# Kernel optimization log

Hardware: AMD Instinct MI355X
Metric: run time of the kernel (lower is better)

## Reference

```python
import jax, jax.numpy as jnp
import numpy as np

N_NODES = 200000
IN_SIZE = 128
OUT_SIZE = 128
N_EDGES = 600000


def setup_inputs() -> dict:
    key = jax.random.key(0)
    k1, k2, k3, k4 = jax.random.split(key, 4)
    embedding = jax.random.normal(k1, (N_NODES, IN_SIZE), dtype=jnp.float32)
    up2down_edge_index = jax.random.randint(k2, (2, N_EDGES), 0, N_NODES, dtype=jnp.int64)
    # GCNConv params (glorot weight, zero bias as in PyG defaults)
    scale = np.sqrt(6.0 / (IN_SIZE + OUT_SIZE)).astype(np.float32)
    W = jax.random.uniform(k3, (IN_SIZE, OUT_SIZE), dtype=jnp.float32, minval=-scale, maxval=scale)
    b = jnp.zeros((OUT_SIZE,), dtype=jnp.float32)
    return {"embedding": embedding, "up2down_edge_index": up2down_edge_index, "W": W, "b": b}


def reference(embedding, up2down_edge_index, W, b):
    # PyG GCNConv: add self-loops, symmetric normalization, linear transform,
    # scatter-sum aggregation, add bias.
    N = embedding.shape[0]
    loops = jnp.arange(N, dtype=up2down_edge_index.dtype)
    src = jnp.concatenate([up2down_edge_index[0], loops])  # message sources
    dst = jnp.concatenate([up2down_edge_index[1], loops])  # message targets

    # degree of each target node (edge_weight = 1)
    deg = jax.ops.segment_sum(jnp.ones_like(src, dtype=embedding.dtype), dst, num_segments=N)
    deg_inv_sqrt = jnp.where(deg > 0, jax.lax.rsqrt(jnp.maximum(deg, 1.0)), 0.0)
    norm = deg_inv_sqrt[src] * deg_inv_sqrt[dst]  # [E+N]

    h = embedding @ W  # [N, out]
    msg = h[src] * norm[:, None]  # gather + scale, [E+N, out]
    out = jax.ops.segment_sum(msg, dst, num_segments=N)  # scatter-add
    return out + b
```

## Files before the change

kernel.cpp:

```cpp
#include <hip/hip_runtime.h>
#include <hip/hip_bf16.h>
#include <stdint.h>

typedef __attribute__((ext_vector_type(8))) short short8v;
typedef __attribute__((ext_vector_type(4))) float f32x4;

__device__ __forceinline__ unsigned short f2bf(float f) {
  unsigned int u = __float_as_uint(f);
  u += 0x7fffu + ((u >> 16) & 1u);
  return (unsigned short)(u >> 16);
}
__device__ __forceinline__ unsigned int pack2bf(float a, float b) {
  return (unsigned int)f2bf(a) | ((unsigned int)f2bf(b) << 16);
}
__device__ __forceinline__ float bf_lo(unsigned int v) { return __uint_as_float(v << 16); }
__device__ __forceinline__ float bf_hi(unsigned int v) { return __uint_as_float(v & 0xffff0000u); }

__global__ void k_count(const int* __restrict__ dst, int* deg, int E) {
  int e = blockIdx.x * blockDim.x + threadIdx.x;
  if (e < E) atomicAdd(&deg[dst[e]], 1);
}

__global__ void k_blocksum(const int* __restrict__ deg, int* partials, float* dis, int N) {
  __shared__ int s[256];
  int t = threadIdx.x;
  int i = blockIdx.x * 256 + t;
  int c = (i < N) ? deg[i] : 0;
  if (i < N) dis[i] = rsqrtf((float)(c + 1));
  s[t] = c;
  __syncthreads();
  for (int off = 128; off > 0; off >>= 1) {
    if (t < off) s[t] += s[t + off];
    __syncthreads();
  }
  if (t == 0) partials[blockIdx.x] = s[0];
}

__global__ void k_scan_partials(int* partials, int nb) {
  __shared__ int s[1024];
  int t = threadIdx.x;
  s[t] = (t < nb) ? partials[t] : 0;
  __syncthreads();
  for (int off = 1; off < 1024; off <<= 1) {
    int v = (t >= off) ? s[t - off] : 0;
    __syncthreads();
    s[t] += v;
    __syncthreads();
  }
  if (t < nb) partials[t] = (t == 0) ? 0 : s[t - 1];
}

__global__ void k_scan_final(const int* __restrict__ deg, const int* __restrict__ partials,
                             int* csr_off, int N, int E) {
  __shared__ int s[256];
  int t = threadIdx.x;
  int i = blockIdx.x * 256 + t;
  int c = (i < N) ? deg[i] : 0;
  s[t] = c;
  __syncthreads();
  for (int off = 1; off < 256; off <<= 1) {
    int v = (t >= off) ? s[t - off] : 0;
    __syncthreads();
    s[t] += v;
    __syncthreads();
  }
  if (i < N) csr_off[i] = partials[blockIdx.x] + s[t] - c;
  if (i == 0) csr_off[N] = E;
}

__global__ void k_fill(const int* __restrict__ src, const int* __restrict__ dst,
                       const int* __restrict__ csr_off, int* cursor, int* csr_src, int E) {
  int e = blockIdx.x * blockDim.x + threadIdx.x;
  if (e < E) {
    int d = dst[e];
    int p = atomicAdd(&cursor[d], 1);
    csr_src[csr_off[d] + p] = src[e];
  }
}

__global__ void k_wprep(const float* __restrict__ W, unsigned short* __restrict__ Wfrag) {
  int t = blockIdx.x * 256 + threadIdx.x;
  int j = t & 7;
  int lane = (t >> 3) & 63;
  int ktct = t >> 9;
  int kt = ktct & 3, ct = ktct >> 2;
  int col = ct * 16 + (lane & 15);
  int k = kt * 32 + 4 * (lane >> 4) + (j & 3) + 16 * (j >> 2);
  Wfrag[t] = f2bf(W[k * 128 + col]);
}

__device__ __forceinline__ short8v pack8(float4 a, float4 b) {
  short8v r;
  r[0] = (short)f2bf(a.x); r[1] = (short)f2bf(a.y);
  r[2] = (short)f2bf(a.z); r[3] = (short)f2bf(a.w);
  r[4] = (short)f2bf(b.x); r[5] = (short)f2bf(b.y);
  r[6] = (short)f2bf(b.z); r[7] = (short)f2bf(b.w);
  return r;
}

__global__ __launch_bounds__(256) void k_gemm3(const float* __restrict__ X,
     const unsigned short* __restrict__ Wfrag, const float* __restrict__ dis,
     unsigned short* __restrict__ hs, int N) {
  __shared__ unsigned short Wl[16384];
  int t = threadIdx.x;
  #pragma unroll
  for (int q = 0; q < 8; ++q)
    ((uint4*)Wl)[q * 256 + t] = ((const uint4*)Wfrag)[q * 256 + t];
  __syncthreads();

  int wv = t >> 6, lane = t & 63;
  int lr = lane & 15, lg = lane >> 4;
  int row = blockIdx.x * 64 + wv * 16 + lr;

  short8v afr[4];
  if (row < N) {
    const float* xp = X + (size_t)row * 128 + 4 * lg;
    #pragma unroll
    for (int kt = 0; kt < 4; ++kt) {
      float4 v0 = *(const float4*)(xp + kt * 32);
      float4 v1 = *(const float4*)(xp + kt * 32 + 16);
      afr[kt] = pack8(v0, v1);
    }
  } else {
    #pragma unroll
    for (int kt = 0; kt < 4; ++kt) {
      float4 z = {0.f, 0.f, 0.f, 0.f};
      afr[kt] = pack8(z, z);
    }
  }
  float d = (row < N) ? dis[row] : 0.f;

  #pragma unroll
  for (int ct = 0; ct < 8; ++ct) {
    f32x4 acc = {0.f, 0.f, 0.f, 0.f};
    #pragma unroll
    for (int kt = 0; kt < 4; ++kt) {
      short8v wfr = *(const short8v*)(Wl + (((ct * 4 + kt) * 64 + lane) * 8));
      acc = __builtin_amdgcn_mfma_f32_16x16x32_bf16(wfr, afr[kt], acc, 0, 0, 0);
    }
    if (row < N) {
      uint2 uu;
      uu.x = pack2bf(acc[0] * d, acc[1] * d);
      uu.y = pack2bf(acc[2] * d, acc[3] * d);
      *(uint2*)(hs + (size_t)row * 128 + ct * 16 + 4 * lg) = uu;
    }
  }
}

__device__ __forceinline__ void acc8(float* a, uint4 g) {
  a[0] += bf_lo(g.x); a[1] += bf_hi(g.x);
  a[2] += bf_lo(g.y); a[3] += bf_hi(g.y);
  a[4] += bf_lo(g.z); a[5] += bf_hi(g.z);
  a[6] += bf_lo(g.w); a[7] += bf_hi(g.w);
}

__global__ __launch_bounds__(256) void k_agg2(const unsigned short* __restrict__ hs_,
     const int* __restrict__ csr_src, const int* __restrict__ csr_off,
     const float* __restrict__ dis, const float* __restrict__ bias,
     float* __restrict__ out, int N) {
  const uint4* hs = (const uint4*)hs_;
  int lane = threadIdx.x & 63;
  int c = lane & 15;
  int base = lane & 48;
  int gid = (blockIdx.x * blockDim.x + threadIdx.x) >> 4;
  int G = (gridDim.x * blockDim.x) >> 4;
  int i0 = (int)(((long long)gid * N) / G);
  int i1 = (int)(((long long)(gid + 1) * N) / G);
  if (i0 >= i1) return;
  float4 bA = ((const float4*)bias)[c * 2];
  float4 bB = ((const float4*)bias)[c * 2 + 1];
  int e1prev = csr_off[i0];
  for (int i = i0; i < i1; ++i) {
    int e0 = e1prev;
    int e1 = csr_off[i + 1];
    e1prev = e1;
    float a[8];
    uint4 sv = hs[(size_t)i * 16 + c];
    a[0] = bf_lo(sv.x); a[1] = bf_hi(sv.x);
    a[2] = bf_lo(sv.y); a[3] = bf_hi(sv.y);
    a[4] = bf_lo(sv.z); a[5] = bf_hi(sv.z);
    a[6] = bf_lo(sv.w); a[7] = bf_hi(sv.w);
    int e = e0;
    while (e < e1) {
      int p = e + c;
      int myidx = (p < e1) ? csr_src[p] : 0;
      int kb = (e1 - e < 16) ? (e1 - e) : 16;
      int k = 0;
      for (; k + 8 <= kb; k += 8) {
        int s[8];
        #pragma unroll
        for (int q = 0; q < 8; ++q) s[q] = __shfl(myidx, base + k + q);
        uint4 g[8];
        #pragma unroll
        for (int q = 0; q < 8; ++q) g[q] = hs[(size_t)s[q] * 16 + c];
        #pragma unroll
        for (int q = 0; q < 8; ++q) acc8(a, g[q]);
      }
      for (; k < kb; k += 4) {
        int s0 = __shfl(myidx, base + k);
        int s1 = __shfl(myidx, base + k + 1);
        int s2 = __shfl(myidx, base + k + 2);
        int s3 = __shfl(myidx, base + k + 3);
        bool v1 = (k + 1 < kb), v2 = (k + 2 < kb), v3 = (k + 3 < kb);
        uint4 g0 = hs[(size_t)s0 * 16 + c];
        uint4 g1 = hs[(size_t)(v1 ? s1 : i) * 16 + c];
        uint4 g2 = hs[(size_t)(v2 ? s2 : i) * 16 + c];
        uint4 g3 = hs[(size_t)(v3 ? s3 : i) * 16 + c];
        if (!v1) { g1.x = g1.y = g1.z = g1.w = 0u; }
        if (!v2) { g2.x = g2.y = g2.z = g2.w = 0u; }
        if (!v3) { g3.x = g3.y = g3.z = g3.w = 0u; }
        acc8(a, g0); acc8(a, g1); acc8(a, g2); acc8(a, g3);
      }
      e += kb;
    }
    float di = dis[i];
    float4 o0, o1;
    o0.x = fmaf(di, a[0], bA.x); o0.y = fmaf(di, a[1], bA.y);
    o0.z = fmaf(di, a[2], bA.z); o0.w = fmaf(di, a[3], bA.w);
    o1.x = fmaf(di, a[4], bB.x); o1.y = fmaf(di, a[5], bB.y);
    o1.z = fmaf(di, a[6], bB.z); o1.w = fmaf(di, a[7], bB.w);
    float4* op = (float4*)(out + (size_t)i * 128);
    op[c * 2] = o0;
    op[c * 2 + 1] = o1;
  }
}

extern "C" void kernel_launch(void* const* d_in, const int* in_sizes, int n_in,
                              void* d_out, int out_size, void* d_ws, size_t ws_size,
                              hipStream_t stream) {
  const float* X    = (const float*)d_in[0];
  const int*   edge = (const int*)d_in[1];
  const float* W    = (const float*)d_in[2];
  const float* bias = (const float*)d_in[3];
  float* out = (float*)d_out;
  int N = in_sizes[0] / 128;
  int E = in_sizes[1] / 2;
  const int* srcArr = edge;
  const int* dstArr = edge + E;

  char* w = (char*)d_ws;
  auto align = [](size_t x) { return (x + 255) & ~(size_t)255; };
  size_t o = 0;
  int*   deg      = (int*)(w + o);   o += align((size_t)N * 4);
  int*   cursor   = (int*)(w + o);   o += align((size_t)N * 4);
  float* dis      = (float*)(w + o); o += align((size_t)N * 4);
  int*   csr_off  = (int*)(w + o);   o += align(((size_t)N + 1) * 4);
  int*   csr_src  = (int*)(w + o);   o += align((size_t)E * 4);
  int*   partials = (int*)(w + o);   o += align((size_t)4096 * 4);
  unsigned short* Wfrag = (unsigned short*)(w + o); o += align((size_t)16384 * 2);
  unsigned short* hs    = (unsigned short*)(w + o);

  int nbN = (N + 255) / 256;
  int nbE = (E + 255) / 256;

  hipMemsetAsync(deg, 0, align((size_t)N * 4) + (size_t)N * 4, stream);
  k_wprep<<<64, 256, 0, stream>>>(W, Wfrag);
  k_count<<<nbE, 256, 0, stream>>>(dstArr, deg, E);
  k_blocksum<<<nbN, 256, 0, stream>>>(deg, partials, dis, N);
  k_scan_partials<<<1, 1024, 0, stream>>>(partials, nbN);
  k_scan_final<<<nbN, 256, 0, stream>>>(deg, partials, csr_off, N, E);
  k_fill<<<nbE, 256, 0, stream>>>(srcArr, dstArr, csr_off, cursor, csr_src, E);
  k_gemm3<<<(N + 63) / 64, 256, 0, stream>>>(X, Wfrag, dis, hs, N);
  k_agg2<<<2048, 256, 0, stream>>>(hs, csr_src, csr_off, dis, bias, out, N);
}
```

Baseline: 163.0 us.

## Persistent register-resident-W GEMM with software prefetch; fuse prep kernels and scans

The GEMM becomes a persistent kernel of 512 blocks. Each wave holds all of W in registers and prefetches the next 16-row X tile while it computes the current one. Output is written as 16-byte stores after a cross-lane shuffle. The memset and W-prep are merged into one kernel, and the single-block partial scan is folded into the final scan kernel, which each block does by summing its preceding partials. This cuts launch count and overlaps X loads with MFMA work, at the cost of heavy register pressure and a redundant partial reduction in every scan block.

New measurement: 151.5 us. 1.08x faster.

```diff
diff --git a/kernel.cpp b/kernel.cpp
--- a/kernel.cpp
+++ b/kernel.cpp
@@ -15,6 +15,27 @@
 }
 __device__ __forceinline__ float bf_lo(unsigned int v) { return __uint_as_float(v << 16); }
 __device__ __forceinline__ float bf_hi(unsigned int v) { return __uint_as_float(v & 0xffff0000u); }
+
+__global__ void k_prep(uint4* __restrict__ zp, int n16,
+                       const float* __restrict__ W, unsigned short* __restrict__ Wfrag) {
+  int b = blockIdx.x;
+  if (b < 64) {
+    int t = b * 256 + threadIdx.x;
+    int j = t & 7;
+    int lane = (t >> 3) & 63;
+    int ktct = t >> 9;
+    int kt = ktct & 3, ct = ktct >> 2;
+    int col = ct * 16 + (lane & 15);
+    int k = kt * 32 + 4 * (lane >> 4) + (j & 3) + 16 * (j >> 2);
+    Wfrag[t] = f2bf(W[k * 128 + col]);
+  } else {
+    int i = (b - 64) * 256 + threadIdx.x;
+    if (i < n16) {
+      uint4 z; z.x = z.y = z.z = z.w = 0u;
+      zp[i] = z;
+    }
+  }
+}
 
 __global__ void k_count(const int* __restrict__ dst, int* deg, int E) {
   int e = blockIdx.x * blockDim.x + threadIdx.x;
@@ -36,24 +57,21 @@
   if (t == 0) partials[blockIdx.x] = s[0];
 }
 
-__global__ void k_scan_partials(int* partials, int nb) {
-  __shared__ int s[1024];
+__global__ void k_scan_final2(const int* __restrict__ deg, const int* __restrict__ partials,
+                              int* csr_off, int N, int E) {
+  __shared__ int s[256];
+  __shared__ int base;
   int t = threadIdx.x;
-  s[t] = (t < nb) ? partials[t] : 0;
+  int accp = 0;
+  for (int j = t; j < blockIdx.x; j += 256) accp += partials[j];
+  s[t] = accp;
   __syncthreads();
-  for (int off = 1; off < 1024; off <<= 1) {
-    int v = (t >= off) ? s[t - off] : 0;
+  for (int off = 128; off > 0; off >>= 1) {
+    if (t < off) s[t] += s[t + off];
     __syncthreads();
-    s[t] += v;
-    __syncthreads();
-  }
-  if (t < nb) partials[t] = (t == 0) ? 0 : s[t - 1];
-}
-
-__global__ void k_scan_final(const int* __restrict__ deg, const int* __restrict__ partials,
-                             int* csr_off, int N, int E) {
-  __shared__ int s[256];
-  int t = threadIdx.x;
+  }
+  if (t == 0) base = s[0];
+  __syncthreads();
   int i = blockIdx.x * 256 + t;
   int c = (i < N) ? deg[i] : 0;
   s[t] = c;
@@ -64,7 +82,7 @@
     s[t] += v;
     __syncthreads();
   }
-  if (i < N) csr_off[i] = partials[blockIdx.x] + s[t] - c;
+  if (i < N) csr_off[i] = base + s[t] - c;
   if (i == 0) csr_off[N] = E;
 }
 
@@ -78,17 +96,6 @@
   }
 }
 
-__global__ void k_wprep(const float* __restrict__ W, unsigned short* __restrict__ Wfrag) {
-  int t = blockIdx.x * 256 + threadIdx.x;
-  int j = t & 7;
-  int lane = (t >> 3) & 63;
-  int ktct = t >> 9;
-  int kt = ktct & 3, ct = ktct >> 2;
-  int col = ct * 16 + (lane & 15);
-  int k = kt * 32 + 4 * (lane >> 4) + (j & 3) + 16 * (j >> 2);
-  Wfrag[t] = f2bf(W[k * 128 + col]);
-}
-
 __device__ __forceinline__ short8v pack8(float4 a, float4 b) {
   short8v r;
   r[0] = (short)f2bf(a.x); r[1] = (short)f2bf(a.y);
@@ -98,52 +105,92 @@
   return r;
 }
 
-__global__ __launch_bounds__(256) void k_gemm3(const float* __restrict__ X,
+
+#define GLOAD(XB, DD, TT, HAS)                                                  \
+  do {                                                                          \
+    if (HAS) {                                                                  \
+      int row_ = (TT) * 16 + lr;                                                \
+      if (row_ < N) {                                                           \
+        const float* xp_ = X + (size_t)row_ * 128 + 4 * lg;                     \
+        _Pragma("unroll") for (int q = 0; q < 4; ++q) {                         \
+          XB[2 * q]     = *(const float4*)(xp_ + q * 32);                       \
+          XB[2 * q + 1] = *(const float4*)(xp_ + q * 32 + 16);                  \
+        }                                                                       \
+        DD = dis[row_];                                                         \
+      } else {                                                                  \
+        _Pragma("unroll") for (int q = 0; q < 8; ++q) {                         \
+          XB[q].x = XB[q].y = XB[q].z = XB[q].w = 0.f;                          \
+        }                                                                       \
+        DD = 0.f;                                                               \
+      }                                                                         \
+    }                                                                           \
+  } while (0)
+
+#define GCOMPUTE(XB, DD, TT)                                                    \
+  do {                                                                          \
+    short8v afr[4];                                                             \
+    _Pragma("unroll") for (int kt = 0; kt < 4; ++kt)                            \
+        afr[kt] = pack8(XB[2 * kt], XB[2 * kt + 1]);                            \
+    int row_ = (TT) * 16 + lr;                                                  \
+    bool wr_ = row_ < N;                                                        \
+    unsigned short* hp_ = hs + (size_t)row_ * 128;                              \
+    float dd_ = DD;                                                             \
+    _Pragma("unroll") for (int cp = 0; cp < 4; ++cp) {                          \
+      f32x4 a0 = {0.f, 0.f, 0.f, 0.f}, a1 = {0.f, 0.f, 0.f, 0.f};               \
+      _Pragma("unroll") for (int kt = 0; kt < 4; ++kt)                          \
+          a0 = __builtin_amdgcn_mfma_f32_16x16x32_bf16(wreg[(2 * cp) * 4 + kt], \
+                                                       afr[kt], a0, 0, 0, 0);   \
+      _Pragma("unroll") for (int kt = 0; kt < 4; ++kt)                          \
+          a1 = __builtin_amdgcn_mfma_f32_16x16x32_bf16(                         \
+              wreg[(2 * cp + 1) * 4 + kt], afr[kt], a1, 0, 0, 0);               \
+      unsigned int u0x = pack2bf(a0[0] * dd_, a0[1] * dd_);                     \
+      unsigned int u0y = pack2bf(a0[2] * dd_, a0[3] * dd_);                     \
+      unsigned int u1x = pack2bf(a1[0] * dd_, a1[1] * dd_);                     \
+      unsigned int u1y = pack2bf(a1[2] * dd_, a1[3] * dd_);                     \
+      int s_ = lg & 1;                                                          \
+      unsigned int sx = s_ ? u0x : u1x, sy = s_ ? u0y : u1y;                    \
+      unsigned int rx = (unsigned int)__shfl_xor((int)sx, 16);                  \
+      unsigned int ry = (unsigned int)__shfl_xor((int)sy, 16);                  \
+      uint4 uu;                                                                 \
+      if (s_ == 0) { uu.x = u0x; uu.y = u0y; uu.z = rx; uu.w = ry; }            \
+      else         { uu.x = rx; uu.y = ry; uu.z = u1x; uu.w = u1y; }            \
+      int cb = (s_ ? (2 * cp + 1) : (2 * cp)) * 16 + 8 * (lg >> 1);             \
+      if (wr_) *(uint4*)(hp_ + cb) = uu;                                        \
+    }                                                                           \
+  } while (0)
+
+__global__ __launch_bounds__(256, 2) void k_gemm5(const float* __restrict__ X,
      const unsigned short* __restrict__ Wfrag, const float* __restrict__ dis,
-     unsigned short* __restrict__ hs, int N) {
-  __shared__ unsigned short Wl[16384];
-  int t = threadIdx.x;
+     unsigned short* __restrict__ hs, int N, int ntile) {
+  int lane = threadIdx.x & 63;
+  int gw = (blockIdx.x * blockDim.x + threadIdx.x) >> 6;
+  int nw = (gridDim.x * blockDim.x) >> 6;
+  int lr = lane & 15, lg = lane >> 4;
+
+  short8v wreg[32];
   #pragma unroll
-  for (int q = 0; q < 8; ++q)
-    ((uint4*)Wl)[q * 256 + t] = ((const uint4*)Wfrag)[q * 256 + t];
-  __syncthreads();
-
-  int wv = t >> 6, lane = t & 63;
-  int lr = lane & 15, lg = lane >> 4;
-  int row = blockIdx.x * 64 + wv * 16 + lr;
-
-  short8v afr[4];
-  if (row < N) {
-    const float* xp = X + (size_t)row * 128 + 4 * lg;
-    #pragma unroll
-    for (int kt = 0; kt < 4; ++kt) {
-      float4 v0 = *(const float4*)(xp + kt * 32);
-      float4 v1 = *(const float4*)(xp + kt * 32 + 16);
-      afr[kt] = pack8(v0, v1);
-    }
-  } else {
-    #pragma unroll
-    for (int kt = 0; kt < 4; ++kt) {
-      float4 z = {0.f, 0.f, 0.f, 0.f};
-      afr[kt] = pack8(z, z);
-    }
-  }
-  float d = (row < N) ? dis[row] : 0.f;
-
-  #pragma unroll
-  for (int ct = 0; ct < 8; ++ct) {
-    f32x4 acc = {0.f, 0.f, 0.f, 0.f};
-    #pragma unroll
-    for (int kt = 0; kt < 4; ++kt) {
-      short8v wfr = *(const short8v*)(Wl + (((ct * 4 + kt) * 64 + lane) * 8));
-      acc = __builtin_amdgcn_mfma_f32_16x16x32_bf16(wfr, afr[kt], acc, 0, 0, 0);
-    }
-    if (row < N) {
-      uint2 uu;
-      uu.x = pack2bf(acc[0] * d, acc[1] * d);
-      uu.y = pack2bf(acc[2] * d, acc[3] * d);
-      *(uint2*)(hs + (size_t)row * 128 + ct * 16 + 4 * lg) = uu;
-    }
+  for (int f = 0; f < 32; ++f)
+    wreg[f] = *(const short8v*)(Wfrag + (size_t)(f * 64 + lane) * 8);
+
+  int tile = gw;
+  if (tile >= ntile) return;
+
+  float4 xv[8], nx[8];
+  float d0 = 0.f, d1 = 0.f;
+  GLOAD(xv, d0, tile, true);
+
+  for (;;) {
+    int t1 = tile + nw;
+    bool h1 = t1 < ntile;
+    GLOAD(nx, d1, t1, h1);
+    GCOMPUTE(xv, d0, tile);
+    if (!h1) break;
+    int t2 = t1 + nw;
+    bool h2 = t2 < ntile;
+    GLOAD(xv, d0, t2, h2);
+    GCOMPUTE(nx, d1, t1);
+    if (!h2) break;
+    tile = t2;
   }
 }
 
@@ -252,14 +299,15 @@
 
   int nbN = (N + 255) / 256;
   int nbE = (E + 255) / 256;
-
-  hipMemsetAsync(deg, 0, align((size_t)N * 4) + (size_t)N * 4, stream);
-  k_wprep<<<64, 256, 0, stream>>>(W, Wfrag);
+  int ntile = (N + 15) / 16;
+
+  size_t zbytes = align((size_t)N * 4) + align((size_t)N * 4);
+  int n16 = (int)(zbytes / 16);
+  k_prep<<<64 + (n16 + 255) / 256, 256, 0, stream>>>((uint4*)deg, n16, W, Wfrag);
   k_count<<<nbE, 256, 0, stream>>>(dstArr, deg, E);
   k_blocksum<<<nbN, 256, 0, stream>>>(deg, partials, dis, N);
-  k_scan_partials<<<1, 1024, 0, stream>>>(partials, nbN);
-  k_scan_final<<<nbN, 256, 0, stream>>>(deg, partials, csr_off, N, E);
+  k_scan_final2<<<nbN, 256, 0, stream>>>(deg, partials, csr_off, N, E);
   k_fill<<<nbE, 256, 0, stream>>>(srcArr, dstArr, csr_off, cursor, csr_src, E);
-  k_gemm3<<<(N + 63) / 64, 256, 0, stream>>>(X, Wfrag, dis, hs, N);
+  k_gemm5<<<512, 256, 0, stream>>>(X, Wfrag, dis, hs, N, ntile);
   k_agg2<<<2048, 256, 0, stream>>>(hs, csr_src, csr_off, dis, bias, out, N);
 }
```
